# Kernel optimization log

Hardware: AMD Instinct MI355X
Metric: run time of the kernel (lower is better)

## Reference

```python
import jax, jax.numpy as jnp
import numpy as np

N_NODES = 100000
N_EDGES = 1600000
F_IN = 128
F_OUT = 128


def _spmm(edge_row, edge_col, edge_weight, X):
    # sparse [N,N] @ dense [N,F]: gather source rows, weight, scatter-add to dest rows
    msgs = edge_weight[:, None] * X[edge_col]  # [E, F]
    return jax.ops.segment_sum(msgs, edge_row, num_segments=N_NODES)


def setup_inputs() -> dict:
    key = jax.random.key(0)
    ks = jax.random.split(key, 7)
    scale = 1.0 / np.sqrt(F_IN)
    return {
        "x": jax.random.normal(ks[0], (N_NODES, F_IN), dtype=jnp.float32),
        "edge_row": jax.random.randint(ks[1], (N_EDGES,), 0, N_NODES, dtype=jnp.int32),
        "edge_col": jax.random.randint(ks[2], (N_EDGES,), 0, N_NODES, dtype=jnp.int32),
        "edge_weight": jax.random.uniform(ks[3], (N_EDGES,), dtype=jnp.float32),
        "w1": jax.random.normal(ks[4], (F_IN, F_IN), dtype=jnp.float32) * scale,
        "w2": jax.random.normal(ks[5], (F_IN, F_OUT), dtype=jnp.float32) * scale,
        "w3": jax.random.normal(ks[6], (F_OUT, F_OUT), dtype=jnp.float32) * scale,
    }


def reference(x, edge_row, edge_col, edge_weight, w1, w2, w3):
    # dropout p=0.0 (eval) -> identity
    h = jax.nn.relu(_spmm(edge_row, edge_col, edge_weight, x @ w1))
    h = jax.nn.relu(_spmm(edge_row, edge_col, edge_weight, h @ w2))
    h = jax.nn.relu(_spmm(edge_row, edge_col, edge_weight, h @ w3))
    return h
```

## Files before the change

### kernel.cpp

```cpp
#include <hip/hip_runtime.h>

#define N_NODES 100000
#define N_EDGES 1600000
#define F 128

#define SCAN_B 1024
#define SCAN_NB ((N_NODES + SCAN_B - 1) / SCAN_B)

#define NSHARD 8
#define SHARD_E (N_EDGES / NSHARD)

#define NCHUNK 256
#define CHUNK_E (N_EDGES / NCHUNK)
#define HALF_N 50000

typedef short bf16x8 __attribute__((ext_vector_type(8)));
typedef float f32x4  __attribute__((ext_vector_type(4)));

union ABFrag {
    bf16x8 v;
    unsigned short u[8];
    uint4  q;
};

__device__ __forceinline__ unsigned short f2bf(float f) {
    unsigned int u = __float_as_uint(f);
    u += 0x7fffu + ((u >> 16) & 1u);
    return (unsigned short)(u >> 16);
}
__device__ __forceinline__ float bflo(unsigned int u) {
    return __uint_as_float(u << 16);
}
__device__ __forceinline__ float bfhi(unsigned int u) {
    return __uint_as_float(u & 0xFFFF0000u);
}


__global__ __launch_bounds__(256) void chunk_hist(
    const int* __restrict__ erow, unsigned char* __restrict__ cb) {
    __shared__ unsigned int h[HALF_N / 4];
    const int c    = blockIdx.x >> 1;
    const int half = blockIdx.x & 1;
    const int t    = threadIdx.x;
    for (int i = t; i < HALF_N / 4; i += 256) h[i] = 0;
    __syncthreads();
    const int lo = half * HALF_N;
    for (int e = c * CHUNK_E + t; e < (c + 1) * CHUNK_E; e += 256) {
        const unsigned int d = (unsigned int)(erow[e] - lo);
        if (d < HALF_N) atomicAdd(&h[d >> 2], 1u << ((d & 3u) * 8u));
    }
    __syncthreads();
    unsigned int* dw = (unsigned int*)(cb + (size_t)c * N_NODES + lo);
    for (int i = t; i < HALF_N / 4; i += 256) dw[i] = h[i];
}

__global__ __launch_bounds__(256) void chunk_prefix(
    unsigned char* __restrict__ cb, int* __restrict__ counts) {
    const int t = blockIdx.x * 256 + threadIdx.x;
    if (t >= (N_NODES / 4) * 8) return;
    const int w   = t >> 3;
    const int sub = t & 7;
    const int c0  = sub * (NCHUNK / 8);
    unsigned int v[NCHUNK / 8];
    unsigned int sum = 0;
#pragma unroll
    for (int j = 0; j < NCHUNK / 8; ++j) {
        v[j] = *(const unsigned int*)(cb + (size_t)(c0 + j) * N_NODES + 4 * (size_t)w);
        sum += v[j];
    }
    unsigned int run = sum;
#pragma unroll
    for (int d = 1; d < 8; d <<= 1) {
        unsigned int tmp = __shfl_up(run, d, 8);
        if (sub >= d) run += tmp;
    }
    unsigned int acc = run - sum;
#pragma unroll
    for (int j = 0; j < NCHUNK / 8; ++j) {
        const unsigned int old = v[j];
        *(unsigned int*)(cb + (size_t)(c0 + j) * N_NODES + 4 * (size_t)w) = acc;
        acc += old;
    }
    if (sub == 7) {
        const int n = w * 4;
        counts[n + 0] = run & 255u;
        counts[n + 1] = (run >> 8) & 255u;
        counts[n + 2] = (run >> 16) & 255u;
        counts[n + 3] = run >> 24;
    }
}

__global__ void scan_block_sums(const int* __restrict__ counts, int* __restrict__ bsums) {
    __shared__ int s[SCAN_B];
    const int t = threadIdx.x;
    const int idx = blockIdx.x * SCAN_B + t;
    int v = (idx < N_NODES) ? counts[idx] : 0;
    s[t] = v;
    __syncthreads();
    for (int off = SCAN_B / 2; off > 0; off >>= 1) {
        if (t < off) s[t] += s[t + off];
        __syncthreads();
    }
    if (t == 0) bsums[blockIdx.x] = s[0];
}

__global__ void scan_bsums(const int* __restrict__ bsums, int* __restrict__ boffs) {
    __shared__ int s[128];
    const int t = threadIdx.x;
    int v = (t < SCAN_NB) ? bsums[t] : 0;
    s[t] = v;
    __syncthreads();
    for (int off = 1; off < 128; off <<= 1) {
        int u = (t >= off) ? s[t - off] : 0;
        __syncthreads();
        s[t] += u;
        __syncthreads();
    }
    if (t < SCAN_NB) boffs[t] = s[t] - v;
}

__global__ void scan_final(const int* __restrict__ counts, const int* __restrict__ boffs,
                           int* __restrict__ row_ptr) {
    __shared__ int s[SCAN_B];
    const int t = threadIdx.x;
    const int idx = blockIdx.x * SCAN_B + t;
    int v = (idx < N_NODES) ? counts[idx] : 0;
    s[t] = v;
    __syncthreads();
    for (int off = 1; off < SCAN_B; off <<= 1) {
        int u = (t >= off) ? s[t - off] : 0;
        __syncthreads();
        s[t] += u;
        __syncthreads();
    }
    if (idx < N_NODES) row_ptr[idx] = boffs[blockIdx.x] + s[t] - v;
    if (idx == 0) row_ptr[N_NODES] = N_EDGES;
}

__global__ __launch_bounds__(256) void chunk_rank(
    const int* __restrict__ erow, const int* __restrict__ ecol,
    const float* __restrict__ ew,
    const unsigned char* __restrict__ cb, const int* __restrict__ row_ptr,
    unsigned long long* __restrict__ rec) {
    __shared__ unsigned int h[HALF_N / 4];
    const int c    = blockIdx.x >> 1;
    const int half = blockIdx.x & 1;
    const int t    = threadIdx.x;
    for (int i = t; i < HALF_N / 4; i += 256) h[i] = 0;
    __syncthreads();
    const int lo = half * HALF_N;
    for (int e = c * CHUNK_E + t; e < (c + 1) * CHUNK_E; e += 256) {
        const int dst = erow[e];
        const unsigned int d = (unsigned int)(dst - lo);
        if (d < HALF_N) {
            const unsigned int old = atomicAdd(&h[d >> 2], 1u << ((d & 3u) * 8u));
            const unsigned int lrank = (old >> ((d & 3u) * 8u)) & 255u;
            const unsigned int pos = (unsigned int)row_ptr[dst]
                                   + (unsigned int)cb[(size_t)c * N_NODES + dst]
                                   + lrank;
            const unsigned int colw = ((unsigned int)ecol[e] << 15)
                                    | (unsigned int)f2bf(ew[e]);
            rec[e] = ((unsigned long long)pos << 32) | colw;
        }
    }
}

__global__ __launch_bounds__(256) void csr_fill_sharded(
    const unsigned long long* __restrict__ rec,
    unsigned int* __restrict__ pairs) {
    const int shard = blockIdx.x & (NSHARD - 1);
    const int e = (blockIdx.x >> 3) * 256 + threadIdx.x;
    const unsigned long long v = rec[e];
    const unsigned int pos = (unsigned int)(v >> 32);
    if ((unsigned int)(pos - (unsigned int)(shard * SHARD_E)) < (unsigned int)SHARD_E) {
        pairs[pos] = (unsigned int)v;
    }
}

__global__ void transpose_w_bf16(const float* __restrict__ W, unsigned short* __restrict__ Wt) {
    const int i = blockIdx.x * 256 + threadIdx.x;
    const int n = i >> 7;
    const int k = i & 127;
    Wt[i] = f2bf(W[k * F + n]);
}

__global__ __launch_bounds__(256) void gemm_mfma(
    const float* __restrict__ Xf,
    const unsigned short* __restrict__ Xb,
    const unsigned short* __restrict__ Wt,
    unsigned short* __restrict__ Y,
    int use_f32_in)
{
    __shared__ unsigned short Wl[4 * 8 * 64 * 8];

    const int tid  = threadIdx.x;
    const int wave = tid >> 6;
    const int lane = tid & 63;

    for (int s = tid; s < 2048; s += 256) {
        const int ln  = s & 63;
        const int ntk = s >> 6;
        const int nt  = ntk & 7;
        const int kt  = ntk >> 3;
        const int n   = nt * 16 + (ln & 15);
        const int k   = kt * 32 + (ln >> 4) * 8;
        *(uint4*)(&Wl[s * 8]) = *(const uint4*)(Wt + n * F + k);
    }
    __syncthreads();

    const int m     = blockIdx.x * 64 + wave * 16 + (lane & 15);
    const bool mval = (m < N_NODES);
    const int kq    = (lane >> 4) * 8;

    f32x4 acc[8] = {};

#pragma unroll
    for (int kt = 0; kt < 4; ++kt) {
        ABFrag a;
        if (mval) {
            if (use_f32_in) {
                const float* p = Xf + (size_t)m * F + kt * 32 + kq;
                const float4 u0 = *(const float4*)p;
                const float4 u1 = *(const float4*)(p + 4);
                a.u[0] = f2bf(u0.x); a.u[1] = f2bf(u0.y);
                a.u[2] = f2bf(u0.z); a.u[3] = f2bf(u0.w);
                a.u[4] = f2bf(u1.x); a.u[5] = f2bf(u1.y);
                a.u[6] = f2bf(u1.z); a.u[7] = f2bf(u1.w);
            } else {
                a.q = *(const uint4*)(Xb + (size_t)m * F + kt * 32 + kq);
#pragma unroll
                for (int j = 0; j < 8; ++j)
                    if (a.u[j] & 0x8000u) a.u[j] = 0;
            }
        } else {
            a.q = make_uint4(0, 0, 0, 0);
        }
#pragma unroll
        for (int nt = 0; nt < 8; ++nt) {
            ABFrag b;
            b.q = *(const uint4*)(&Wl[((kt * 8 + nt) * 64 + lane) * 8]);
            acc[nt] = __builtin_amdgcn_mfma_f32_16x16x32_bf16(a.v, b.v, acc[nt], 0, 0, 0);
        }
    }

    const int rbase = blockIdx.x * 64 + wave * 16 + (lane >> 4) * 4;
    const int cbase = lane & 15;
#pragma unroll
    for (int r = 0; r < 4; ++r) {
        const int row = rbase + r;
        if (row < N_NODES) {
#pragma unroll
            for (int nt = 0; nt < 8; ++nt) {
                Y[(size_t)row * F + nt * 16 + cbase] = f2bf(acc[nt][r]);
            }
        }
    }
}

__global__ __launch_bounds__(256) void spmm_csr_bf16(
    const unsigned short* __restrict__ Xb,
    const int* __restrict__ row_ptr,
    const unsigned int* __restrict__ pairs,
    unsigned short* __restrict__ Ob,
    float* __restrict__ Of,
    int final_mode) {
    const int tid = threadIdx.x;
    const int l16 = tid & 15;
    const int q   = tid >> 4;
    const int row = blockIdx.x * 16 + q;

    const int beg = row_ptr[row];
    const int end = row_ptr[row + 1];

    float a[8] = {};
    int i = beg;
    for (; i + 1 < end; i += 2) {
        const unsigned int p0 = pairs[i], p1 = pairs[i + 1];
        const uint4 v0 = *(const uint4*)(Xb + (size_t)(p0 >> 15) * F + l16 * 8);
        const uint4 v1 = *(const uint4*)(Xb + (size_t)(p1 >> 15) * F + l16 * 8);
        const float w0 = bflo(p0 & 0x7FFFu);
        const float w1 = bflo(p1 & 0x7FFFu);
        a[0] += w0 * bflo(v0.x); a[1] += w0 * bfhi(v0.x);
        a[2] += w0 * bflo(v0.y); a[3] += w0 * bfhi(v0.y);
        a[4] += w0 * bflo(v0.z); a[5] += w0 * bfhi(v0.z);
        a[6] += w0 * bflo(v0.w); a[7] += w0 * bfhi(v0.w);
        a[0] += w1 * bflo(v1.x); a[1] += w1 * bfhi(v1.x);
        a[2] += w1 * bflo(v1.y); a[3] += w1 * bfhi(v1.y);
        a[4] += w1 * bflo(v1.z); a[5] += w1 * bfhi(v1.z);
        a[6] += w1 * bflo(v1.w); a[7] += w1 * bfhi(v1.w);
    }
    if (i < end) {
        const unsigned int p0 = pairs[i];
        const uint4 v0 = *(const uint4*)(Xb + (size_t)(p0 >> 15) * F + l16 * 8);
        const float w0 = bflo(p0 & 0x7FFFu);
        a[0] += w0 * bflo(v0.x); a[1] += w0 * bfhi(v0.x);
        a[2] += w0 * bflo(v0.y); a[3] += w0 * bfhi(v0.y);
        a[4] += w0 * bflo(v0.z); a[5] += w0 * bfhi(v0.z);
        a[6] += w0 * bflo(v0.w); a[7] += w0 * bfhi(v0.w);
    }

    if (final_mode) {
        float4 o0 = {fmaxf(a[0], 0.f), fmaxf(a[1], 0.f), fmaxf(a[2], 0.f), fmaxf(a[3], 0.f)};
        float4 o1 = {fmaxf(a[4], 0.f), fmaxf(a[5], 0.f), fmaxf(a[6], 0.f), fmaxf(a[7], 0.f)};
        float* p = Of + (size_t)row * F + l16 * 8;
        *(float4*)p = o0;
        *(float4*)(p + 4) = o1;
    } else {
        uint4 o;
        o.x = (unsigned int)f2bf(a[0]) | ((unsigned int)f2bf(a[1]) << 16);
        o.y = (unsigned int)f2bf(a[2]) | ((unsigned int)f2bf(a[3]) << 16);
        o.z = (unsigned int)f2bf(a[4]) | ((unsigned int)f2bf(a[5]) << 16);
        o.w = (unsigned int)f2bf(a[6]) | ((unsigned int)f2bf(a[7]) << 16);
        *(uint4*)(Ob + (size_t)row * F + l16 * 8) = o;
    }
}


extern "C" void kernel_launch(void* const* d_in, const int* in_sizes, int n_in,
                              void* d_out, int out_size, void* d_ws, size_t ws_size,
                              hipStream_t stream) {
    const float* x    = (const float*)d_in[0];
    const int*   erow = (const int*)d_in[1];
    const int*   ecol = (const int*)d_in[2];
    const float* ew   = (const float*)d_in[3];
    const float* w1   = (const float*)d_in[4];
    const float* w2   = (const float*)d_in[5];
    const float* w3   = (const float*)d_in[6];
    float* out = (float*)d_out;

    char* ws = (char*)d_ws;
    size_t off = 0;
    auto alloc = [&](size_t bytes) -> char* {
        char* p = ws + off;
        off += (bytes + 255) & ~(size_t)255;
        return p;
    };
    unsigned short* bufA = (unsigned short*)alloc((size_t)N_NODES * F * 2);
    unsigned short* bufB = (unsigned short*)alloc((size_t)N_NODES * F * 2);
    unsigned int* pairs  = (unsigned int*)alloc((size_t)N_EDGES * 4);
    int* counts  = (int*)alloc((size_t)N_NODES * sizeof(int));
    int* row_ptr = (int*)alloc(((size_t)N_NODES + 1) * sizeof(int));
    int* bsums   = (int*)alloc((size_t)SCAN_NB * sizeof(int));
    int* boffs   = (int*)alloc((size_t)SCAN_NB * sizeof(int));
    unsigned short* wt1 = (unsigned short*)alloc((size_t)F * F * 2);
    unsigned short* wt2 = (unsigned short*)alloc((size_t)F * F * 2);
    unsigned short* wt3 = (unsigned short*)alloc((size_t)F * F * 2);

    unsigned char* cb = (unsigned char*)bufA;
    unsigned long long* rec = (unsigned long long*)bufB;

    chunk_hist<<<NCHUNK * 2, 256, 0, stream>>>(erow, cb);
    chunk_prefix<<<((N_NODES / 4) * 8 + 255) / 256, 256, 0, stream>>>(cb, counts);
    scan_block_sums<<<SCAN_NB, SCAN_B, 0, stream>>>(counts, bsums);
    scan_bsums<<<1, 128, 0, stream>>>(bsums, boffs);
    scan_final<<<SCAN_NB, SCAN_B, 0, stream>>>(counts, boffs, row_ptr);
    chunk_rank<<<NCHUNK * 2, 256, 0, stream>>>(erow, ecol, ew, cb, row_ptr, rec);
    csr_fill_sharded<<<(N_EDGES / 256) * NSHARD, 256, 0, stream>>>(rec, pairs);

    transpose_w_bf16<<<64, 256, 0, stream>>>(w1, wt1);
    transpose_w_bf16<<<64, 256, 0, stream>>>(w2, wt2);
    transpose_w_bf16<<<64, 256, 0, stream>>>(w3, wt3);

    const int ggrid = (N_NODES + 63) / 64;
    const int sgrid = N_NODES / 16;

    gemm_mfma<<<ggrid, 256, 0, stream>>>(x, nullptr, wt1, bufA, 1);
    spmm_csr_bf16<<<sgrid, 256, 0, stream>>>(bufA, row_ptr, pairs, bufB, nullptr, 0);
    gemm_mfma<<<ggrid, 256, 0, stream>>>(nullptr, bufB, wt2, bufA, 0);
    spmm_csr_bf16<<<sgrid, 256, 0, stream>>>(bufA, row_ptr, pairs, bufB, nullptr, 0);
    gemm_mfma<<<ggrid, 256, 0, stream>>>(nullptr, bufB, wt3, bufA, 0);
    spmm_csr_bf16<<<sgrid, 256, 0, stream>>>(bufA, row_ptr, pairs, nullptr, out, 1);
}
```

Measured before the change: 449.5 us.

## Fuse SpMM aggregation with following dense GEMM via LDS tile

The intermediate SpMM kernels now apply ReLU, stage their 16x128 bf16 output tile in shared memory, and immediately multiply it by the next layer's weight with MFMA before writing. This removes two standalone GEMM launches and the global round trip of the intermediate activations. Each 16-row block now reads W (32KB) from global/L2 per block, and adds a block-level sync in the gather kernel.

```diff
diff --git a/kernel.cpp b/kernel.cpp
--- a/kernel.cpp
+++ b/kernel.cpp
@@ -186,10 +186,8 @@
 
 __global__ __launch_bounds__(256) void gemm_mfma(
     const float* __restrict__ Xf,
-    const unsigned short* __restrict__ Xb,
     const unsigned short* __restrict__ Wt,
-    unsigned short* __restrict__ Y,
-    int use_f32_in)
+    unsigned short* __restrict__ Y)
 {
     __shared__ unsigned short Wl[4 * 8 * 64 * 8];
 
@@ -218,20 +216,13 @@
     for (int kt = 0; kt < 4; ++kt) {
         ABFrag a;
         if (mval) {
-            if (use_f32_in) {
-                const float* p = Xf + (size_t)m * F + kt * 32 + kq;
-                const float4 u0 = *(const float4*)p;
-                const float4 u1 = *(const float4*)(p + 4);
-                a.u[0] = f2bf(u0.x); a.u[1] = f2bf(u0.y);
-                a.u[2] = f2bf(u0.z); a.u[3] = f2bf(u0.w);
-                a.u[4] = f2bf(u1.x); a.u[5] = f2bf(u1.y);
-                a.u[6] = f2bf(u1.z); a.u[7] = f2bf(u1.w);
-            } else {
-                a.q = *(const uint4*)(Xb + (size_t)m * F + kt * 32 + kq);
-#pragma unroll
-                for (int j = 0; j < 8; ++j)
-                    if (a.u[j] & 0x8000u) a.u[j] = 0;
-            }
+            const float* p = Xf + (size_t)m * F + kt * 32 + kq;
+            const float4 u0 = *(const float4*)p;
+            const float4 u1 = *(const float4*)(p + 4);
+            a.u[0] = f2bf(u0.x); a.u[1] = f2bf(u0.y);
+            a.u[2] = f2bf(u0.z); a.u[3] = f2bf(u0.w);
+            a.u[4] = f2bf(u1.x); a.u[5] = f2bf(u1.y);
+            a.u[6] = f2bf(u1.z); a.u[7] = f2bf(u1.w);
         } else {
             a.q = make_uint4(0, 0, 0, 0);
         }
@@ -257,13 +248,15 @@
     }
 }
 
-__global__ __launch_bounds__(256) void spmm_csr_bf16(
+__global__ __launch_bounds__(256) void spmm_gemm_fused(
     const unsigned short* __restrict__ Xb,
     const int* __restrict__ row_ptr,
     const unsigned int* __restrict__ pairs,
-    unsigned short* __restrict__ Ob,
-    float* __restrict__ Of,
-    int final_mode) {
+    const unsigned short* __restrict__ Wt,
+    unsigned short* __restrict__ Y)
+{
+    __shared__ unsigned short Al[16][136];
+
     const int tid = threadIdx.x;
     const int l16 = tid & 15;
     const int q   = tid >> 4;
@@ -299,20 +292,89 @@
         a[6] += w0 * bflo(v0.w); a[7] += w0 * bfhi(v0.w);
     }
 
-    if (final_mode) {
-        float4 o0 = {fmaxf(a[0], 0.f), fmaxf(a[1], 0.f), fmaxf(a[2], 0.f), fmaxf(a[3], 0.f)};
-        float4 o1 = {fmaxf(a[4], 0.f), fmaxf(a[5], 0.f), fmaxf(a[6], 0.f), fmaxf(a[7], 0.f)};
-        float* p = Of + (size_t)row * F + l16 * 8;
-        *(float4*)p = o0;
-        *(float4*)(p + 4) = o1;
-    } else {
-        uint4 o;
-        o.x = (unsigned int)f2bf(a[0]) | ((unsigned int)f2bf(a[1]) << 16);
-        o.y = (unsigned int)f2bf(a[2]) | ((unsigned int)f2bf(a[3]) << 16);
-        o.z = (unsigned int)f2bf(a[4]) | ((unsigned int)f2bf(a[5]) << 16);
-        o.w = (unsigned int)f2bf(a[6]) | ((unsigned int)f2bf(a[7]) << 16);
-        *(uint4*)(Ob + (size_t)row * F + l16 * 8) = o;
-    }
+    uint4 o;
+    o.x = (unsigned int)f2bf(fmaxf(a[0], 0.f)) | ((unsigned int)f2bf(fmaxf(a[1], 0.f)) << 16);
+    o.y = (unsigned int)f2bf(fmaxf(a[2], 0.f)) | ((unsigned int)f2bf(fmaxf(a[3], 0.f)) << 16);
+    o.z = (unsigned int)f2bf(fmaxf(a[4], 0.f)) | ((unsigned int)f2bf(fmaxf(a[5], 0.f)) << 16);
+    o.w = (unsigned int)f2bf(fmaxf(a[6], 0.f)) | ((unsigned int)f2bf(fmaxf(a[7], 0.f)) << 16);
+    *(uint4*)(&Al[q][l16 * 8]) = o;
+    __syncthreads();
+
+    const int wave = tid >> 6;
+    const int lane = tid & 63;
+    const int kq   = (lane >> 4) * 8;
+    const int arow = lane & 15;
+
+    f32x4 acc[2] = {};
+#pragma unroll
+    for (int kt = 0; kt < 4; ++kt) {
+        ABFrag af;
+        af.q = *(const uint4*)(&Al[arow][kt * 32 + kq]);
+#pragma unroll
+        for (int nt = 0; nt < 2; ++nt) {
+            const int n = wave * 32 + nt * 16 + (lane & 15);
+            ABFrag bf_;
+            bf_.q = *(const uint4*)(Wt + n * F + kt * 32 + kq);
+            acc[nt] = __builtin_amdgcn_mfma_f32_16x16x32_bf16(af.v, bf_.v, acc[nt], 0, 0, 0);
+        }
+    }
+
+    const int rbase = blockIdx.x * 16 + (lane >> 4) * 4;
+    const int cbase = wave * 32 + (lane & 15);
+#pragma unroll
+    for (int nt = 0; nt < 2; ++nt) {
+#pragma unroll
+        for (int r = 0; r < 4; ++r) {
+            Y[(size_t)(rbase + r) * F + cbase + nt * 16] = f2bf(acc[nt][r]);
+        }
+    }
+}
+
+__global__ __launch_bounds__(256) void spmm_csr_final(
+    const unsigned short* __restrict__ Xb,
+    const int* __restrict__ row_ptr,
+    const unsigned int* __restrict__ pairs,
+    float* __restrict__ Of) {
+    const int tid = threadIdx.x;
+    const int l16 = tid & 15;
+    const int q   = tid >> 4;
+    const int row = blockIdx.x * 16 + q;
+
+    const int beg = row_ptr[row];
+    const int end = row_ptr[row + 1];
+
+    float a[8] = {};
+    int i = beg;
+    for (; i + 1 < end; i += 2) {
+        const unsigned int p0 = pairs[i], p1 = pairs[i + 1];
+        const uint4 v0 = *(const uint4*)(Xb + (size_t)(p0 >> 15) * F + l16 * 8);
+        const uint4 v1 = *(const uint4*)(Xb + (size_t)(p1 >> 15) * F + l16 * 8);
+        const float w0 = bflo(p0 & 0x7FFFu);
+        const float w1 = bflo(p1 & 0x7FFFu);
+        a[0] += w0 * bflo(v0.x); a[1] += w0 * bfhi(v0.x);
+        a[2] += w0 * bflo(v0.y); a[3] += w0 * bfhi(v0.y);
+        a[4] += w0 * bflo(v0.z); a[5] += w0 * bfhi(v0.z);
+        a[6] += w0 * bflo(v0.w); a[7] += w0 * bfhi(v0.w);
+        a[0] += w1 * bflo(v1.x); a[1] += w1 * bfhi(v1.x);
+        a[2] += w1 * bflo(v1.y); a[3] += w1 * bfhi(v1.y);
+        a[4] += w1 * bflo(v1.z); a[5] += w1 * bfhi(v1.z);
+        a[6] += w1 * bflo(v1.w); a[7] += w1 * bfhi(v1.w);
+    }
+    if (i < end) {
+        const unsigned int p0 = pairs[i];
+        const uint4 v0 = *(const uint4*)(Xb + (size_t)(p0 >> 15) * F + l16 * 8);
+        const float w0 = bflo(p0 & 0x7FFFu);
+        a[0] += w0 * bflo(v0.x); a[1] += w0 * bfhi(v0.x);
+        a[2] += w0 * bflo(v0.y); a[3] += w0 * bfhi(v0.y);
+        a[4] += w0 * bflo(v0.z); a[5] += w0 * bfhi(v0.z);
+        a[6] += w0 * bflo(v0.w); a[7] += w0 * bfhi(v0.w);
+    }
+
+    float4 o0 = {fmaxf(a[0], 0.f), fmaxf(a[1], 0.f), fmaxf(a[2], 0.f), fmaxf(a[3], 0.f)};
+    float4 o1 = {fmaxf(a[4], 0.f), fmaxf(a[5], 0.f), fmaxf(a[6], 0.f), fmaxf(a[7], 0.f)};
+    float* p = Of + (size_t)row * F + l16 * 8;
+    *(float4*)p = o0;
+    *(float4*)(p + 4) = o1;
 }
 
 
@@ -364,10 +426,8 @@
     const int ggrid = (N_NODES + 63) / 64;
     const int sgrid = N_NODES / 16;
 
-    gemm_mfma<<<ggrid, 256, 0, stream>>>(x, nullptr, wt1, bufA, 1);
-    spmm_csr_bf16<<<sgrid, 256, 0, stream>>>(bufA, row_ptr, pairs, bufB, nullptr, 0);
-    gemm_mfma<<<ggrid, 256, 0, stream>>>(nullptr, bufB, wt2, bufA, 0);
-    spmm_csr_bf16<<<sgrid, 256, 0, stream>>>(bufA, row_ptr, pairs, bufB, nullptr, 0);
-    gemm_mfma<<<ggrid, 256, 0, stream>>>(nullptr, bufB, wt3, bufA, 0);
-    spmm_csr_bf16<<<sgrid, 256, 0, stream>>>(bufA, row_ptr, pairs, nullptr, out, 1);
-}
+    gemm_mfma<<<ggrid, 256, 0, stream>>>(x, wt1, bufA);
+    spmm_gemm_fused<<<sgrid, 256, 0, stream>>>(bufA, row_ptr, pairs, wt2, bufB);
+    spmm_gemm_fused<<<sgrid, 256, 0, stream>>>(bufB, row_ptr, pairs, wt3, bufA);
+    spmm_csr_final<<<sgrid, 256, 0, stream>>>(bufA, row_ptr, pairs, out);
+}
```

New measurement: 450.0 us. About the same (+0.1%).

## Store activations in column-sliced layout and run SpMM per slice with thread-per-row

Applied to the files above, without the earlier changes.

Intermediate bf16 activations are stored as 8 column slices of 16 features each, node-major within a slice. The SpMM now assigns one thread per row per slice, with 8 slice blocks per row group. Each thread gathers 32-byte rows from one slice, so the gather working set per slice fits better in cache. ReLU moves into the SpMM output instead of being applied on the next GEMM's input, the three weight transposes merge into one launch, and pairs loads and outputs use nontemporal hints. In exchange, each row's CSR index list is reread 8 times, and thread-per-row parallelism can leave lanes idle on rows with uneven degree.

```diff
diff --git a/kernel.cpp b/kernel.cpp
--- a/kernel.cpp
+++ b/kernel.cpp
@@ -14,8 +14,14 @@
 #define CHUNK_E (N_EDGES / NCHUNK)
 #define HALF_N 50000
 
+#define NSLICE 8
+#define SLICE_C 16
+#define SROWS 256
+#define SBLK ((N_NODES + SROWS - 1) / SROWS)
+
 typedef short bf16x8 __attribute__((ext_vector_type(8)));
 typedef float f32x4  __attribute__((ext_vector_type(4)));
+typedef unsigned int u32x4 __attribute__((ext_vector_type(4)));
 
 union ABFrag {
     bf16x8 v;
@@ -177,19 +183,26 @@
     }
 }
 
-__global__ void transpose_w_bf16(const float* __restrict__ W, unsigned short* __restrict__ Wt) {
-    const int i = blockIdx.x * 256 + threadIdx.x;
+__global__ void transpose_w_bf16(const float* __restrict__ W1,
+                                 const float* __restrict__ W2,
+                                 const float* __restrict__ W3,
+                                 unsigned short* __restrict__ Wt1,
+                                 unsigned short* __restrict__ Wt2,
+                                 unsigned short* __restrict__ Wt3) {
+    const int g = blockIdx.x >> 6;
+    const int i = (blockIdx.x & 63) * 256 + threadIdx.x;
     const int n = i >> 7;
     const int k = i & 127;
+    const float* W = (g == 0) ? W1 : (g == 1) ? W2 : W3;
+    unsigned short* Wt = (g == 0) ? Wt1 : (g == 1) ? Wt2 : Wt3;
     Wt[i] = f2bf(W[k * F + n]);
 }
+
 
 __global__ __launch_bounds__(256) void gemm_mfma(
     const float* __restrict__ Xf,
-    const unsigned short* __restrict__ Xb,
     const unsigned short* __restrict__ Wt,
-    unsigned short* __restrict__ Y,
-    int use_f32_in)
+    unsigned short* __restrict__ Ysl)
 {
     __shared__ unsigned short Wl[4 * 8 * 64 * 8];
 
@@ -218,20 +231,13 @@
     for (int kt = 0; kt < 4; ++kt) {
         ABFrag a;
         if (mval) {
-            if (use_f32_in) {
-                const float* p = Xf + (size_t)m * F + kt * 32 + kq;
-                const float4 u0 = *(const float4*)p;
-                const float4 u1 = *(const float4*)(p + 4);
-                a.u[0] = f2bf(u0.x); a.u[1] = f2bf(u0.y);
-                a.u[2] = f2bf(u0.z); a.u[3] = f2bf(u0.w);
-                a.u[4] = f2bf(u1.x); a.u[5] = f2bf(u1.y);
-                a.u[6] = f2bf(u1.z); a.u[7] = f2bf(u1.w);
-            } else {
-                a.q = *(const uint4*)(Xb + (size_t)m * F + kt * 32 + kq);
-#pragma unroll
-                for (int j = 0; j < 8; ++j)
-                    if (a.u[j] & 0x8000u) a.u[j] = 0;
-            }
+            const float* p = Xf + (size_t)m * F + kt * 32 + kq;
+            const float4 u0 = *(const float4*)p;
+            const float4 u1 = *(const float4*)(p + 4);
+            a.u[0] = f2bf(u0.x); a.u[1] = f2bf(u0.y);
+            a.u[2] = f2bf(u0.z); a.u[3] = f2bf(u0.w);
+            a.u[4] = f2bf(u1.x); a.u[5] = f2bf(u1.y);
+            a.u[6] = f2bf(u1.z); a.u[7] = f2bf(u1.w);
         } else {
             a.q = make_uint4(0, 0, 0, 0);
         }
@@ -251,67 +257,159 @@
         if (row < N_NODES) {
 #pragma unroll
             for (int nt = 0; nt < 8; ++nt) {
-                Y[(size_t)row * F + nt * 16 + cbase] = f2bf(acc[nt][r]);
+                Ysl[((size_t)nt * N_NODES + row) * SLICE_C + cbase] = f2bf(acc[nt][r]);
             }
         }
     }
 }
 
-__global__ __launch_bounds__(256) void spmm_csr_bf16(
-    const unsigned short* __restrict__ Xb,
+__global__ __launch_bounds__(256) void gemm_mfma_sl(
+    const unsigned short* __restrict__ Asl,
+    const unsigned short* __restrict__ Wt,
+    unsigned short* __restrict__ Ysl)
+{
+    __shared__ unsigned short Wl[4 * 8 * 64 * 8];
+
+    const int tid  = threadIdx.x;
+    const int wave = tid >> 6;
+    const int lane = tid & 63;
+
+    for (int s = tid; s < 2048; s += 256) {
+        const int ln  = s & 63;
+        const int ntk = s >> 6;
+        const int nt  = ntk & 7;
+        const int kt  = ntk >> 3;
+        const int n   = nt * 16 + (ln & 15);
+        const int k   = kt * 32 + (ln >> 4) * 8;
+        *(uint4*)(&Wl[s * 8]) = *(const uint4*)(Wt + n * F + k);
+    }
+    __syncthreads();
+
+    const int m     = blockIdx.x * 64 + wave * 16 + (lane & 15);
+    const bool mval = (m < N_NODES);
+    const int kq    = (lane >> 4) * 8;
+
+    f32x4 acc[8] = {};
+
+#pragma unroll
+    for (int kt = 0; kt < 4; ++kt) {
+        ABFrag a;
+        if (mval) {
+            const int c = kt * 32 + kq;
+            a.q = *(const uint4*)(Asl + ((size_t)(c >> 4) * N_NODES + m) * SLICE_C + (c & 15));
+        } else {
+            a.q = make_uint4(0, 0, 0, 0);
+        }
+#pragma unroll
+        for (int nt = 0; nt < 8; ++nt) {
+            ABFrag b;
+            b.q = *(const uint4*)(&Wl[((kt * 8 + nt) * 64 + lane) * 8]);
+            acc[nt] = __builtin_amdgcn_mfma_f32_16x16x32_bf16(a.v, b.v, acc[nt], 0, 0, 0);
+        }
+    }
+
+    const int rbase = blockIdx.x * 64 + wave * 16 + (lane >> 4) * 4;
+    const int cbase = lane & 15;
+#pragma unroll
+    for (int r = 0; r < 4; ++r) {
+        const int row = rbase + r;
+        if (row < N_NODES) {
+#pragma unroll
+            for (int nt = 0; nt < 8; ++nt) {
+                Ysl[((size_t)nt * N_NODES + row) * SLICE_C + cbase] = f2bf(acc[nt][r]);
+            }
+        }
+    }
+}
+
+__global__ __launch_bounds__(256) void spmm_sliced(
+    const unsigned short* __restrict__ Xsl,
     const int* __restrict__ row_ptr,
     const unsigned int* __restrict__ pairs,
-    unsigned short* __restrict__ Ob,
+    unsigned short* __restrict__ Ysl,
     float* __restrict__ Of,
-    int final_mode) {
-    const int tid = threadIdx.x;
-    const int l16 = tid & 15;
-    const int q   = tid >> 4;
-    const int row = blockIdx.x * 16 + q;
-
+    int final_mode)
+{
+    const int sl  = blockIdx.x & (NSLICE - 1);
+    const int row = (blockIdx.x >> 3) * SROWS + threadIdx.x;
+    if (row >= N_NODES) return;
+
+    const unsigned short* Xs = Xsl + (size_t)sl * N_NODES * SLICE_C;
     const int beg = row_ptr[row];
     const int end = row_ptr[row + 1];
 
-    float a[8] = {};
+    float a[16] = {};
     int i = beg;
     for (; i + 1 < end; i += 2) {
-        const unsigned int p0 = pairs[i], p1 = pairs[i + 1];
-        const uint4 v0 = *(const uint4*)(Xb + (size_t)(p0 >> 15) * F + l16 * 8);
-        const uint4 v1 = *(const uint4*)(Xb + (size_t)(p1 >> 15) * F + l16 * 8);
+        const unsigned int p0 = __builtin_nontemporal_load(pairs + i);
+        const unsigned int p1 = __builtin_nontemporal_load(pairs + i + 1);
+        const unsigned short* r0 = Xs + (size_t)(p0 >> 15) * SLICE_C;
+        const unsigned short* r1 = Xs + (size_t)(p1 >> 15) * SLICE_C;
+        const uint4 u0 = *(const uint4*)r0;
+        const uint4 u1 = *(const uint4*)(r0 + 8);
+        const uint4 u2 = *(const uint4*)r1;
+        const uint4 u3 = *(const uint4*)(r1 + 8);
         const float w0 = bflo(p0 & 0x7FFFu);
         const float w1 = bflo(p1 & 0x7FFFu);
-        a[0] += w0 * bflo(v0.x); a[1] += w0 * bfhi(v0.x);
-        a[2] += w0 * bflo(v0.y); a[3] += w0 * bfhi(v0.y);
-        a[4] += w0 * bflo(v0.z); a[5] += w0 * bfhi(v0.z);
-        a[6] += w0 * bflo(v0.w); a[7] += w0 * bfhi(v0.w);
-        a[0] += w1 * bflo(v1.x); a[1] += w1 * bfhi(v1.x);
-        a[2] += w1 * bflo(v1.y); a[3] += w1 * bfhi(v1.y);
-        a[4] += w1 * bflo(v1.z); a[5] += w1 * bfhi(v1.z);
-        a[6] += w1 * bflo(v1.w); a[7] += w1 * bfhi(v1.w);
+        a[0]  += w0 * bflo(u0.x); a[1]  += w0 * bfhi(u0.x);
+        a[2]  += w0 * bflo(u0.y); a[3]  += w0 * bfhi(u0.y);
+        a[4]  += w0 * bflo(u0.z); a[5]  += w0 * bfhi(u0.z);
+        a[6]  += w0 * bflo(u0.w); a[7]  += w0 * bfhi(u0.w);
+        a[8]  += w0 * bflo(u1.x); a[9]  += w0 * bfhi(u1.x);
+        a[10] += w0 * bflo(u1.y); a[11] += w0 * bfhi(u1.y);
+        a[12] += w0 * bflo(u1.z); a[13] += w0 * bfhi(u1.z);
+        a[14] += w0 * bflo(u1.w); a[15] += w0 * bfhi(u1.w);
+        a[0]  += w1 * bflo(u2.x); a[1]  += w1 * bfhi(u2.x);
+        a[2]  += w1 * bflo(u2.y); a[3]  += w1 * bfhi(u2.y);
+        a[4]  += w1 * bflo(u2.z); a[5]  += w1 * bfhi(u2.z);
+        a[6]  += w1 * bflo(u2.w); a[7]  += w1 * bfhi(u2.w);
+        a[8]  += w1 * bflo(u3.x); a[9]  += w1 * bfhi(u3.x);
+        a[10] += w1 * bflo(u3.y); a[11] += w1 * bfhi(u3.y);
+        a[12] += w1 * bflo(u3.z); a[13] += w1 * bfhi(u3.z);
+        a[14] += w1 * bflo(u3.w); a[15] += w1 * bfhi(u3.w);
     }
     if (i < end) {
-        const unsigned int p0 = pairs[i];
-        const uint4 v0 = *(const uint4*)(Xb + (size_t)(p0 >> 15) * F + l16 * 8);
+        const unsigned int p0 = __builtin_nontemporal_load(pairs + i);
+        const unsigned short* r0 = Xs + (size_t)(p0 >> 15) * SLICE_C;
+        const uint4 u0 = *(const uint4*)r0;
+        const uint4 u1 = *(const uint4*)(r0 + 8);
         const float w0 = bflo(p0 & 0x7FFFu);
-        a[0] += w0 * bflo(v0.x); a[1] += w0 * bfhi(v0.x);
-        a[2] += w0 * bflo(v0.y); a[3] += w0 * bfhi(v0.y);
-        a[4] += w0 * bflo(v0.z); a[5] += w0 * bfhi(v0.z);
-        a[6] += w0 * bflo(v0.w); a[7] += w0 * bfhi(v0.w);
-    }
+        a[0]  += w0 * bflo(u0.x); a[1]  += w0 * bfhi(u0.x);
+        a[2]  += w0 * bflo(u0.y); a[3]  += w0 * bfhi(u0.y);
+        a[4]  += w0 * bflo(u0.z); a[5]  += w0 * bfhi(u0.z);
+        a[6]  += w0 * bflo(u0.w); a[7]  += w0 * bfhi(u0.w);
+        a[8]  += w0 * bflo(u1.x); a[9]  += w0 * bfhi(u1.x);
+        a[10] += w0 * bflo(u1.y); a[11] += w0 * bfhi(u1.y);
+        a[12] += w0 * bflo(u1.z); a[13] += w0 * bfhi(u1.z);
+        a[14] += w0 * bflo(u1.w); a[15] += w0 * bfhi(u1.w);
+    }
+
+#pragma unroll
+    for (int j = 0; j < 16; ++j) a[j] = fmaxf(a[j], 0.f);
 
     if (final_mode) {
-        float4 o0 = {fmaxf(a[0], 0.f), fmaxf(a[1], 0.f), fmaxf(a[2], 0.f), fmaxf(a[3], 0.f)};
-        float4 o1 = {fmaxf(a[4], 0.f), fmaxf(a[5], 0.f), fmaxf(a[6], 0.f), fmaxf(a[7], 0.f)};
-        float* p = Of + (size_t)row * F + l16 * 8;
-        *(float4*)p = o0;
-        *(float4*)(p + 4) = o1;
+        float* p = Of + (size_t)row * F + sl * SLICE_C;
+        f32x4 o0 = {a[0], a[1], a[2], a[3]};
+        f32x4 o1 = {a[4], a[5], a[6], a[7]};
+        f32x4 o2 = {a[8], a[9], a[10], a[11]};
+        f32x4 o3 = {a[12], a[13], a[14], a[15]};
+        __builtin_nontemporal_store(o0, (f32x4*)p);
+        __builtin_nontemporal_store(o1, (f32x4*)(p + 4));
+        __builtin_nontemporal_store(o2, (f32x4*)(p + 8));
+        __builtin_nontemporal_store(o3, (f32x4*)(p + 12));
     } else {
-        uint4 o;
-        o.x = (unsigned int)f2bf(a[0]) | ((unsigned int)f2bf(a[1]) << 16);
-        o.y = (unsigned int)f2bf(a[2]) | ((unsigned int)f2bf(a[3]) << 16);
-        o.z = (unsigned int)f2bf(a[4]) | ((unsigned int)f2bf(a[5]) << 16);
-        o.w = (unsigned int)f2bf(a[6]) | ((unsigned int)f2bf(a[7]) << 16);
-        *(uint4*)(Ob + (size_t)row * F + l16 * 8) = o;
+        unsigned short* y = Ysl + ((size_t)sl * N_NODES + row) * SLICE_C;
+        u32x4 o0, o1;
+        o0.x = (unsigned int)f2bf(a[0])  | ((unsigned int)f2bf(a[1])  << 16);
+        o0.y = (unsigned int)f2bf(a[2])  | ((unsigned int)f2bf(a[3])  << 16);
+        o0.z = (unsigned int)f2bf(a[4])  | ((unsigned int)f2bf(a[5])  << 16);
+        o0.w = (unsigned int)f2bf(a[6])  | ((unsigned int)f2bf(a[7])  << 16);
+        o1.x = (unsigned int)f2bf(a[8])  | ((unsigned int)f2bf(a[9])  << 16);
+        o1.y = (unsigned int)f2bf(a[10]) | ((unsigned int)f2bf(a[11]) << 16);
+        o1.z = (unsigned int)f2bf(a[12]) | ((unsigned int)f2bf(a[13]) << 16);
+        o1.w = (unsigned int)f2bf(a[14]) | ((unsigned int)f2bf(a[15]) << 16);
+        __builtin_nontemporal_store(o0, (u32x4*)y);
+        __builtin_nontemporal_store(o1, (u32x4*)(y + 8));
     }
 }
 
@@ -357,17 +455,15 @@
     chunk_rank<<<NCHUNK * 2, 256, 0, stream>>>(erow, ecol, ew, cb, row_ptr, rec);
     csr_fill_sharded<<<(N_EDGES / 256) * NSHARD, 256, 0, stream>>>(rec, pairs);
 
-    transpose_w_bf16<<<64, 256, 0, stream>>>(w1, wt1);
-    transpose_w_bf16<<<64, 256, 0, stream>>>(w2, wt2);
-    transpose_w_bf16<<<64, 256, 0, stream>>>(w3, wt3);
+    transpose_w_bf16<<<192, 256, 0, stream>>>(w1, w2, w3, wt1, wt2, wt3);
 
     const int ggrid = (N_NODES + 63) / 64;
-    const int sgrid = N_NODES / 16;
-
-    gemm_mfma<<<ggrid, 256, 0, stream>>>(x, nullptr, wt1, bufA, 1);
-    spmm_csr_bf16<<<sgrid, 256, 0, stream>>>(bufA, row_ptr, pairs, bufB, nullptr, 0);
-    gemm_mfma<<<ggrid, 256, 0, stream>>>(nullptr, bufB, wt2, bufA, 0);
-    spmm_csr_bf16<<<sgrid, 256, 0, stream>>>(bufA, row_ptr, pairs, bufB, nullptr, 0);
-    gemm_mfma<<<ggrid, 256, 0, stream>>>(nullptr, bufB, wt3, bufA, 0);
-    spmm_csr_bf16<<<sgrid, 256, 0, stream>>>(bufA, row_ptr, pairs, nullptr, out, 1);
-}
+    const int sgrid = NSLICE * SBLK;
+
+    gemm_mfma<<<ggrid, 256, 0, stream>>>(x, wt1, bufA);
+    spmm_sliced<<<sgrid, 256, 0, stream>>>(bufA, row_ptr, pairs, bufB, nullptr, 0);
+    gemm_mfma_sl<<<ggrid, 256, 0, stream>>>(bufB, wt2, bufA);
+    spmm_sliced<<<sgrid, 256, 0, stream>>>(bufA, row_ptr, pairs, bufB, nullptr, 0);
+    gemm_mfma_sl<<<ggrid, 256, 0, stream>>>(bufB, wt3, bufA);
+    spmm_sliced<<<sgrid, 256, 0, stream>>>(bufA, row_ptr, pairs, nullptr, out, 1);
+}
```

Result: slower. 745.1 us (+65.8%).
